# Kernel optimization log

Measured on AMD Instinct MI355X. Metric: run time of the kernel, lower is better.

## Reference

```python
import jax, jax.numpy as jnp
import numpy as np

B, D, H, NE = 16, 64, 768, 7  # batch, max_doc_len, bert hidden, n_emotion
FEAT = H + NE + 1             # 776; pair dim = 2*FEAT = 1552

def setup_inputs() -> dict:
    key = jax.random.key(0)
    ks = jax.random.split(key, 8)
    s = lambda k, shp, fan: jax.random.normal(k, shp, jnp.float32) / np.sqrt(fan)
    return {
        "pooled_output": jax.random.normal(ks[0], (B * D, H), jnp.float32),
        "speaker_ids": jax.random.randint(ks[1], (B, D), 0, 2, jnp.int64),
        "emo_w": s(ks[2], (H, NE), H),
        "emo_b": jnp.zeros((NE,), jnp.float32),
        "gate_w": s(ks[3], (2 * FEAT, 2), 2 * FEAT),
        "gate_b": jnp.zeros((2,), jnp.float32),
        "exp_w1": s(ks[4], (2, 2 * FEAT, 256), 2 * FEAT),
        "exp_b1": jnp.zeros((2, 256), jnp.float32),
        "exp_w2": s(ks[5], (2, 256, 2), 256),
        "exp_b2": jnp.zeros((2, 2), jnp.float32),
    }

def reference(pooled_output, speaker_ids, emo_w, emo_b, gate_w, gate_b, exp_w1, exp_b1, exp_w2, exp_b2):
    # emotion head (dropout is identity in eval)
    emotion_pred = pooled_output @ emo_w + emo_b                      # [B*D, 7]
    # concatenated per-utterance embedding [B, D, FEAT]
    spk = speaker_ids.reshape(-1, 1).astype(pooled_output.dtype)
    conc = jnp.concatenate([pooled_output, emotion_pred, spk], axis=1).reshape(B, D, FEAT)
    # vectorized pair build: (t, end_t) with t <= end_t, end_t-major order
    idx_end, idx_t = np.tril_indices(D)                               # P = D*(D+1)/2
    pair = jnp.concatenate([conc[:, idx_t], conc[:, idx_end]], axis=-1)  # [B, P, 2*FEAT]
    flat = pair.reshape(-1, 2 * FEAT)                                 # [N, 1552]
    # gating (detached input, guiding_lambda = 0 so no subtask label term)
    gating = jax.lax.stop_gradient(flat) @ gate_w + gate_b            # [N, 2]
    # soft-gated expert combine
    h = jnp.einsum('nf,efh->enh', flat, exp_w1) + exp_b1[:, None, :]  # [E, N, 256]
    o = jnp.einsum('enh,ehc->enc', h, exp_w2) + exp_b2[:, None, :]    # [E, N, 2]
    cause_pred = jnp.einsum('enc,ne->nc', o, gating)                  # [N, 2]
    return emotion_pred, cause_pred
```

## Files before the change

kernel.cpp:

```cpp
#include <hip/hip_runtime.h>


#define NE_    7
#define H_     768
#define FEAT_  776
#define NROW   1024
#define PAIRS  2080
#define KP     800
#define BTJ    12
#define NBATCH 16

typedef float f32x4 __attribute__((ext_vector_type(4)));
typedef short bf16x8 __attribute__((ext_vector_type(8)));

__device__ __forceinline__ unsigned short f2b(float x) {
    unsigned u = __float_as_uint(x);
    u += 0x7FFFu + ((u >> 16) & 1u);
    return (unsigned short)(u >> 16);
}

__global__ __launch_bounds__(1024) void kPrep(
        const float* __restrict__ pooled,
        const float* __restrict__ emo_w,
        const float* __restrict__ emo_b,
        const float* __restrict__ gate_w,
        const float* __restrict__ w1,
        const float* __restrict__ b1,
        const float* __restrict__ w2,
        const float* __restrict__ b2,
        float* __restrict__ out,
        unsigned short* __restrict__ wsBt,
        float* __restrict__ wsbc) {
    const int blk = blockIdx.x;
    const int tid = threadIdx.x;
    const int l   = tid & 63;
    const int wv  = tid >> 6;

    if (blk < 64) {
        const int row = blk * 16 + wv;
        const float* pr = pooled + (size_t)row * H_;
        float acc[NE_] = {0.f, 0.f, 0.f, 0.f, 0.f, 0.f, 0.f};
#pragma unroll
        for (int i = 0; i < 12; ++i) {
            const float p = pr[l + 64 * i];
            const float* ew = emo_w + (size_t)(l + 64 * i) * NE_;
#pragma unroll
            for (int k = 0; k < NE_; ++k) acc[k] += p * ew[k];
        }
#pragma unroll
        for (int off = 32; off; off >>= 1)
#pragma unroll
            for (int k = 0; k < NE_; ++k) acc[k] += __shfl_down(acc[k], off);
        if (l == 0) {
#pragma unroll
            for (int k = 0; k < NE_; ++k)
                out[(size_t)row * NE_ + k] = acc[k] + emo_b[k];
        }
        return;
    }

    if (blk < 258) {
        const int mr = (blk - 64) * 16 + wv;
        const int e = mr / 1552, rr = mr - e * 1552;
        const float4 a = ((const float4*)(w1 + ((size_t)e * 1552 + rr) * 256))[l];
        const float4* wvp = (const float4*)(w2 + (size_t)e * 512);
        const float4 q0 = wvp[l * 2], q1 = wvp[l * 2 + 1];
        float a0 = a.x * q0.x + a.y * q0.z + a.z * q1.x + a.w * q1.z;
        float a1 = a.x * q0.y + a.y * q0.w + a.z * q1.y + a.w * q1.w;
#pragma unroll
        for (int off = 32; off; off >>= 1) {
            a0 += __shfl_down(a0, off);
            a1 += __shfl_down(a1, off);
        }
        if (l == 0) {
            const int half = rr / FEAT_, f = rr - half * FEAT_;
            const int j = half * 4 + e * 2;
            wsBt[j * KP + f]       = f2b(a0);
            wsBt[(j + 1) * KP + f] = f2b(a1);
        }
        return;
    }

    if (wv < 2) {
        const int e = wv;
        const float4 a = ((const float4*)(b1 + e * 256))[l];
        const float4* wvp = (const float4*)(w2 + (size_t)e * 512);
        const float4 q0 = wvp[l * 2], q1 = wvp[l * 2 + 1];
        float a0 = a.x * q0.x + a.y * q0.z + a.z * q1.x + a.w * q1.z;
        float a1 = a.x * q0.y + a.y * q0.w + a.z * q1.y + a.w * q1.w;
#pragma unroll
        for (int off = 32; off; off >>= 1) {
            a0 += __shfl_down(a0, off);
            a1 += __shfl_down(a1, off);
        }
        if (l == 0) {
            wsbc[e * 2]     = a0 + b2[e * 2];
            wsbc[e * 2 + 1] = a1 + b2[e * 2 + 1];
        }
    }
    for (int gi = tid; gi < 3104; gi += 1024) {
        const int half = gi / 1552, r2 = gi - half * 1552, f = r2 >> 1, c = r2 & 1;
        wsBt[(8 + half * 2 + c) * KP + f] =
            f2b(gate_w[((size_t)half * FEAT_ + f) * 2 + c]);
    }
    for (int z = tid; z < BTJ * 24; z += 1024) {
        const int j = z / 24, f = FEAT_ + z % 24;
        wsBt[j * KP + f] = 0;
    }
}

__global__ __launch_bounds__(1024) void kProj(
        const float* __restrict__ pooled,
        const int*   __restrict__ spk,
        const float* __restrict__ gate_b,
        const unsigned short* __restrict__ wsBt,
        const float* __restrict__ wsbc,
        float* __restrict__ out) {
    const int b   = blockIdx.x;
    const int tid = threadIdx.x;
    const int l   = tid & 63;
    const int wv  = tid >> 6;

    __shared__ float part[4 * 64 * 16];

    const int R0 = b * 64;
    const int m = wv & 3, kq = wv >> 2, g = l >> 4, n = l & 15;
    const int arow = R0 + m * 16 + n;
    const int kt0 = (kq == 0) ? 0 : (1 + 6 * kq);
    const int cnt = (kq == 0) ? 7 : 6;

    bf16x8 af[7];
#pragma unroll
    for (int s = 0; s < 7; ++s) {
        bf16x8 t = {0, 0, 0, 0, 0, 0, 0, 0};
        if (s < cnt) {
            const int k0 = (kt0 + s) * 32 + g * 8;
            if (k0 < H_) {
                const float4 u0 = *(const float4*)(pooled + (size_t)arow * H_ + k0);
                const float4 u1 = *(const float4*)(pooled + (size_t)arow * H_ + k0 + 4);
                t[0] = (short)f2b(u0.x); t[1] = (short)f2b(u0.y);
                t[2] = (short)f2b(u0.z); t[3] = (short)f2b(u0.w);
                t[4] = (short)f2b(u1.x); t[5] = (short)f2b(u1.y);
                t[6] = (short)f2b(u1.z); t[7] = (short)f2b(u1.w);
            }
        }
        af[s] = t;
    }
    if (kq == 3 && g == 0) {
        bf16x8 t;
        t[0] = (short)f2b(out[(size_t)arow * NE_ + 0]);
        t[1] = (short)f2b(out[(size_t)arow * NE_ + 1]);
        t[2] = (short)f2b(out[(size_t)arow * NE_ + 2]);
        t[3] = (short)f2b(out[(size_t)arow * NE_ + 3]);
        t[4] = (short)f2b(out[(size_t)arow * NE_ + 4]);
        t[5] = (short)f2b(out[(size_t)arow * NE_ + 5]);
        t[6] = (short)f2b(out[(size_t)arow * NE_ + 6]);
        t[7] = (short)f2b((float)spk[arow]);
        af[5] = t;
    }

    f32x4 acc = {0.f, 0.f, 0.f, 0.f};
#pragma unroll
    for (int s = 0; s < 7; ++s) {
        if (s < cnt) {
            const int k0 = (kt0 + s) * 32 + g * 8;
            bf16x8 bfr = {0, 0, 0, 0, 0, 0, 0, 0};
            if (n < BTJ)
                bfr = *(const bf16x8*)(wsBt + n * KP + k0);
            acc = __builtin_amdgcn_mfma_f32_16x16x32_bf16(af[s], bfr, acc, 0, 0, 0);
        }
    }
#pragma unroll
    for (int i = 0; i < 4; ++i)
        part[(kq * 64 + m * 16 + g * 4 + i) * 16 + n] = acc[i];
    __syncthreads();

    {
        const int r = tid >> 4, c = tid & 15;
        const float v = part[r * 16 + c] + part[(64 + r) * 16 + c] +
                        part[(128 + r) * 16 + c] + part[(192 + r) * 16 + c];
        part[r * 16 + c] = v;
    }
    __syncthreads();

    const float bc0 = wsbc[0], bc1 = wsbc[1], bc2 = wsbc[2], bc3 = wsbc[3];
    const float gb0 = gate_b[0], gb1 = gate_b[1];
    float* oc = out + (size_t)NROW * NE_ + (size_t)b * PAIRS * 2;
    for (int p = tid; p < PAIRS; p += 1024) {
        int end = (int)((sqrtf(8.0f * (float)p + 1.0f) - 1.0f) * 0.5f);
        while ((end + 1) * (end + 2) / 2 <= p) end++;
        while (end * (end + 1) / 2 > p) end--;
        const int tt = p - end * (end + 1) / 2;
        const float* pt = part + tt * 16;
        const float* pe = part + end * 16;
        const float g0 = pt[8] + pe[10] + gb0;
        const float g1 = pt[9] + pe[11] + gb1;
        oc[p * 2]     = (pt[0] + pe[4] + bc0) * g0 + (pt[2] + pe[6] + bc2) * g1;
        oc[p * 2 + 1] = (pt[1] + pe[5] + bc1) * g0 + (pt[3] + pe[7] + bc3) * g1;
    }
}

extern "C" void kernel_launch(void* const* d_in, const int* in_sizes, int n_in,
                              void* d_out, int out_size, void* d_ws, size_t ws_size,
                              hipStream_t stream) {
    const float* pooled = (const float*)d_in[0];
    const int*   spk    = (const int*)d_in[1];
    const float* emo_w  = (const float*)d_in[2];
    const float* emo_b  = (const float*)d_in[3];
    const float* gate_w = (const float*)d_in[4];
    const float* gate_b = (const float*)d_in[5];
    const float* exp_w1 = (const float*)d_in[6];
    const float* exp_b1 = (const float*)d_in[7];
    const float* exp_w2 = (const float*)d_in[8];
    const float* exp_b2 = (const float*)d_in[9];

    float* out = (float*)d_out;
    unsigned short* wsBt = (unsigned short*)d_ws;
    float* wsbc = (float*)((char*)d_ws + BTJ * KP * 2);

    hipLaunchKernelGGL(kPrep, dim3(259), dim3(1024), 0, stream,
                       pooled, emo_w, emo_b, gate_w,
                       exp_w1, exp_b1, exp_w2, exp_b2, out, wsBt, wsbc);
    hipLaunchKernelGGL(kProj, dim3(NBATCH), dim3(1024), 0, stream,
                       pooled, spk, gate_b, wsBt, wsbc, out);
}
```

Before: 19.99 us.

## Fuse prep and projection kernels using a global atomic producer-consumer barrier

```diff
diff --git a/kernel.cpp b/kernel.cpp
--- a/kernel.cpp
+++ b/kernel.cpp
@@ -9,6 +9,14 @@
 #define KP     800
 #define BTJ    12
 #define NBATCH 16
+#define NMBLK  194
+#define MISCB  194
+#define NPROD  195
+#define CONS0  195
+#define NBLKS  211
+
+__device__ int g_arr = 0;
+__device__ int g_dep = 0;
 
 typedef float f32x4 __attribute__((ext_vector_type(4)));
 typedef short bf16x8 __attribute__((ext_vector_type(8)));
@@ -19,48 +27,31 @@
     return (unsigned short)(u >> 16);
 }
 
-__global__ __launch_bounds__(1024) void kPrep(
+__device__ __forceinline__ void st_agent(float* p, float v) {
+    __hip_atomic_store(p, v, __ATOMIC_RELAXED, __HIP_MEMORY_SCOPE_AGENT);
+}
+
+__global__ __launch_bounds__(1024) void kOne(
         const float* __restrict__ pooled,
+        const int*   __restrict__ spk,
         const float* __restrict__ emo_w,
         const float* __restrict__ emo_b,
         const float* __restrict__ gate_w,
+        const float* __restrict__ gate_b,
         const float* __restrict__ w1,
         const float* __restrict__ b1,
         const float* __restrict__ w2,
         const float* __restrict__ b2,
         float* __restrict__ out,
-        unsigned short* __restrict__ wsBt,
+        float* __restrict__ wsBt,
         float* __restrict__ wsbc) {
     const int blk = blockIdx.x;
     const int tid = threadIdx.x;
     const int l   = tid & 63;
     const int wv  = tid >> 6;
 
-    if (blk < 64) {
-        const int row = blk * 16 + wv;
-        const float* pr = pooled + (size_t)row * H_;
-        float acc[NE_] = {0.f, 0.f, 0.f, 0.f, 0.f, 0.f, 0.f};
-#pragma unroll
-        for (int i = 0; i < 12; ++i) {
-            const float p = pr[l + 64 * i];
-            const float* ew = emo_w + (size_t)(l + 64 * i) * NE_;
-#pragma unroll
-            for (int k = 0; k < NE_; ++k) acc[k] += p * ew[k];
-        }
-#pragma unroll
-        for (int off = 32; off; off >>= 1)
-#pragma unroll
-            for (int k = 0; k < NE_; ++k) acc[k] += __shfl_down(acc[k], off);
-        if (l == 0) {
-#pragma unroll
-            for (int k = 0; k < NE_; ++k)
-                out[(size_t)row * NE_ + k] = acc[k] + emo_b[k];
-        }
-        return;
-    }
-
-    if (blk < 258) {
-        const int mr = (blk - 64) * 16 + wv;
+    if (blk < NMBLK) {
+        const int mr = blk * 16 + wv;
         const int e = mr / 1552, rr = mr - e * 1552;
         const float4 a = ((const float4*)(w1 + ((size_t)e * 1552 + rr) * 256))[l];
         const float4* wvp = (const float4*)(w2 + (size_t)e * 512);
@@ -75,55 +66,51 @@
         if (l == 0) {
             const int half = rr / FEAT_, f = rr - half * FEAT_;
             const int j = half * 4 + e * 2;
-            wsBt[j * KP + f]       = f2b(a0);
-            wsBt[(j + 1) * KP + f] = f2b(a1);
-        }
+            st_agent(wsBt + j * KP + f, a0);
+            st_agent(wsBt + (j + 1) * KP + f, a1);
+        }
+        __syncthreads();
+        if (tid == 0) atomicAdd(&g_arr, 1);
         return;
     }
 
-    if (wv < 2) {
-        const int e = wv;
-        const float4 a = ((const float4*)(b1 + e * 256))[l];
-        const float4* wvp = (const float4*)(w2 + (size_t)e * 512);
-        const float4 q0 = wvp[l * 2], q1 = wvp[l * 2 + 1];
-        float a0 = a.x * q0.x + a.y * q0.z + a.z * q1.x + a.w * q1.z;
-        float a1 = a.x * q0.y + a.y * q0.w + a.z * q1.y + a.w * q1.w;
-#pragma unroll
-        for (int off = 32; off; off >>= 1) {
-            a0 += __shfl_down(a0, off);
-            a1 += __shfl_down(a1, off);
-        }
-        if (l == 0) {
-            wsbc[e * 2]     = a0 + b2[e * 2];
-            wsbc[e * 2 + 1] = a1 + b2[e * 2 + 1];
-        }
-    }
-    for (int gi = tid; gi < 3104; gi += 1024) {
-        const int half = gi / 1552, r2 = gi - half * 1552, f = r2 >> 1, c = r2 & 1;
-        wsBt[(8 + half * 2 + c) * KP + f] =
-            f2b(gate_w[((size_t)half * FEAT_ + f) * 2 + c]);
-    }
-    for (int z = tid; z < BTJ * 24; z += 1024) {
-        const int j = z / 24, f = FEAT_ + z % 24;
-        wsBt[j * KP + f] = 0;
-    }
-}
-
-__global__ __launch_bounds__(1024) void kProj(
-        const float* __restrict__ pooled,
-        const int*   __restrict__ spk,
-        const float* __restrict__ gate_b,
-        const unsigned short* __restrict__ wsBt,
-        const float* __restrict__ wsbc,
-        float* __restrict__ out) {
-    const int b   = blockIdx.x;
-    const int tid = threadIdx.x;
-    const int l   = tid & 63;
-    const int wv  = tid >> 6;
-
-    __shared__ float part[4 * 64 * 16];
-
-    const int R0 = b * 64;
+    if (blk == MISCB) {
+        if (wv < 2) {
+            const int e = wv;
+            const float4 a = ((const float4*)(b1 + e * 256))[l];
+            const float4* wvp = (const float4*)(w2 + (size_t)e * 512);
+            const float4 q0 = wvp[l * 2], q1 = wvp[l * 2 + 1];
+            float a0 = a.x * q0.x + a.y * q0.z + a.z * q1.x + a.w * q1.z;
+            float a1 = a.x * q0.y + a.y * q0.w + a.z * q1.y + a.w * q1.w;
+#pragma unroll
+            for (int off = 32; off; off >>= 1) {
+                a0 += __shfl_down(a0, off);
+                a1 += __shfl_down(a1, off);
+            }
+            if (l == 0) {
+                st_agent(wsbc + e * 2,     a0 + b2[e * 2]);
+                st_agent(wsbc + e * 2 + 1, a1 + b2[e * 2 + 1]);
+            }
+        }
+        for (int gi = tid; gi < 3104; gi += 1024) {
+            const int half = gi / 1552, r2 = gi - half * 1552, f = r2 >> 1, c = r2 & 1;
+            st_agent(wsBt + (8 + half * 2 + c) * KP + f,
+                     gate_w[((size_t)half * FEAT_ + f) * 2 + c]);
+        }
+        for (int z = tid; z < BTJ * 24; z += 1024) {
+            const int j = z / 24, f = FEAT_ + z % 24;
+            st_agent(wsBt + j * KP + f, 0.0f);
+        }
+        __syncthreads();
+        if (tid == 0) atomicAdd(&g_arr, 1);
+        return;
+    }
+
+    const int b = blk - CONS0, R0 = b * 64;
+    __shared__ __align__(16) short sBt[BTJ * KP];
+    __shared__ float emoL[64][8];
+    __shared__ float part[4096];
+
     const int m = wv & 3, kq = wv >> 2, g = l >> 4, n = l & 15;
     const int arow = R0 + m * 16 + n;
     const int kt0 = (kq == 0) ? 0 : (1 + 6 * kq);
@@ -146,18 +133,67 @@
         }
         af[s] = t;
     }
+
+#pragma unroll
+    for (int r4 = 0; r4 < 4; ++r4) {
+        const int lr = wv * 4 + r4;
+        const float* pr = pooled + (size_t)(R0 + lr) * H_;
+        float acc[NE_] = {0.f, 0.f, 0.f, 0.f, 0.f, 0.f, 0.f};
+#pragma unroll
+        for (int i = 0; i < 12; ++i) {
+            const float p = pr[l + 64 * i];
+            const float* ew = emo_w + (size_t)(l + 64 * i) * NE_;
+#pragma unroll
+            for (int k = 0; k < NE_; ++k) acc[k] += p * ew[k];
+        }
+#pragma unroll
+        for (int off = 32; off; off >>= 1)
+#pragma unroll
+            for (int k = 0; k < NE_; ++k) acc[k] += __shfl_down(acc[k], off);
+        if (l == 0) {
+#pragma unroll
+            for (int k = 0; k < NE_; ++k) {
+                const float v = acc[k] + emo_b[k];
+                out[(size_t)(R0 + lr) * NE_ + k] = v;
+                emoL[lr][k] = v;
+            }
+            emoL[lr][7] = (float)spk[R0 + lr];
+        }
+    }
+    __syncthreads();
+
     if (kq == 3 && g == 0) {
+        const int lr = m * 16 + n;
         bf16x8 t;
-        t[0] = (short)f2b(out[(size_t)arow * NE_ + 0]);
-        t[1] = (short)f2b(out[(size_t)arow * NE_ + 1]);
-        t[2] = (short)f2b(out[(size_t)arow * NE_ + 2]);
-        t[3] = (short)f2b(out[(size_t)arow * NE_ + 3]);
-        t[4] = (short)f2b(out[(size_t)arow * NE_ + 4]);
-        t[5] = (short)f2b(out[(size_t)arow * NE_ + 5]);
-        t[6] = (short)f2b(out[(size_t)arow * NE_ + 6]);
-        t[7] = (short)f2b((float)spk[arow]);
+        t[0] = (short)f2b(emoL[lr][0]); t[1] = (short)f2b(emoL[lr][1]);
+        t[2] = (short)f2b(emoL[lr][2]); t[3] = (short)f2b(emoL[lr][3]);
+        t[4] = (short)f2b(emoL[lr][4]); t[5] = (short)f2b(emoL[lr][5]);
+        t[6] = (short)f2b(emoL[lr][6]); t[7] = (short)f2b(emoL[lr][7]);
         af[5] = t;
     }
+
+    if (tid == 0) {
+        int guard = 0;
+        while (__hip_atomic_load(&g_arr, __ATOMIC_RELAXED, __HIP_MEMORY_SCOPE_AGENT) < NPROD
+               && ++guard < (1 << 20))
+            __builtin_amdgcn_s_sleep(2);
+    }
+    __syncthreads();
+    if (tid == 0) {
+        const int d = atomicAdd(&g_dep, 1);
+        if (d == NBATCH - 1) {
+            __hip_atomic_store(&g_arr, 0, __ATOMIC_RELAXED, __HIP_MEMORY_SCOPE_AGENT);
+            __hip_atomic_store(&g_dep, 0, __ATOMIC_RELAXED, __HIP_MEMORY_SCOPE_AGENT);
+        }
+    }
+
+    for (int i = tid; i < BTJ * KP / 2; i += 1024) {
+        const unsigned long long v = __hip_atomic_load(
+            (const unsigned long long*)wsBt + i, __ATOMIC_RELAXED, __HIP_MEMORY_SCOPE_AGENT);
+        sBt[i * 2]     = (short)f2b(__uint_as_float((unsigned)v));
+        sBt[i * 2 + 1] = (short)f2b(__uint_as_float((unsigned)(v >> 32)));
+    }
+    __syncthreads();
 
     f32x4 acc = {0.f, 0.f, 0.f, 0.f};
 #pragma unroll
@@ -166,7 +202,7 @@
             const int k0 = (kt0 + s) * 32 + g * 8;
             bf16x8 bfr = {0, 0, 0, 0, 0, 0, 0, 0};
             if (n < BTJ)
-                bfr = *(const bf16x8*)(wsBt + n * KP + k0);
+                bfr = *(const bf16x8*)(sBt + n * KP + k0);
             acc = __builtin_amdgcn_mfma_f32_16x16x32_bf16(af[s], bfr, acc, 0, 0, 0);
         }
     }
@@ -183,7 +219,14 @@
     }
     __syncthreads();
 
-    const float bc0 = wsbc[0], bc1 = wsbc[1], bc2 = wsbc[2], bc3 = wsbc[3];
+    const unsigned long long c01 = __hip_atomic_load(
+        (const unsigned long long*)wsbc, __ATOMIC_RELAXED, __HIP_MEMORY_SCOPE_AGENT);
+    const unsigned long long c23 = __hip_atomic_load(
+        (const unsigned long long*)wsbc + 1, __ATOMIC_RELAXED, __HIP_MEMORY_SCOPE_AGENT);
+    const float bc0 = __uint_as_float((unsigned)c01);
+    const float bc1 = __uint_as_float((unsigned)(c01 >> 32));
+    const float bc2 = __uint_as_float((unsigned)c23);
+    const float bc3 = __uint_as_float((unsigned)(c23 >> 32));
     const float gb0 = gate_b[0], gb1 = gate_b[1];
     float* oc = out + (size_t)NROW * NE_ + (size_t)b * PAIRS * 2;
     for (int p = tid; p < PAIRS; p += 1024) {
@@ -214,13 +257,11 @@
     const float* exp_w2 = (const float*)d_in[8];
     const float* exp_b2 = (const float*)d_in[9];
 
-    float* out = (float*)d_out;
-    unsigned short* wsBt = (unsigned short*)d_ws;
-    float* wsbc = (float*)((char*)d_ws + BTJ * KP * 2);
-
-    hipLaunchKernelGGL(kPrep, dim3(259), dim3(1024), 0, stream,
-                       pooled, emo_w, emo_b, gate_w,
+    float* out  = (float*)d_out;
+    float* wsBt = (float*)d_ws;
+    float* wsbc = wsBt + BTJ * KP;
+
+    hipLaunchKernelGGL(kOne, dim3(NBLKS), dim3(1024), 0, stream,
+                       pooled, spk, emo_w, emo_b, gate_w, gate_b,
                        exp_w1, exp_b1, exp_w2, exp_b2, out, wsBt, wsbc);
-    hipLaunchKernelGGL(kProj, dim3(NBATCH), dim3(1024), 0, stream,
-                       pooled, spk, gate_b, wsBt, wsbc, out);
-}
+}
```

Result: slower. 37.97 us (+89.9%).
